# Optimization experiments

Measured on AMD Instinct MI355X. Metric: run time of the kernel, lower is better.

Reference implementation:

```python
import jax, jax.numpy as jnp
import numpy as np

EPS = 1e-5

def _ln(x, g, b):
    mu = jnp.mean(x, axis=-1, keepdims=True)
    var = jnp.var(x, axis=-1, keepdims=True)
    return (x - mu) * jax.lax.rsqrt(var + EPS) * g + b

def setup_inputs() -> dict:
    key = jax.random.key(0)
    ks = jax.random.split(key, 8)
    B, L, D, H = 2, 2048, 1024, 16
    F = 4096
    s = 0.02
    return {
        "x": jax.random.normal(ks[0], (B, L, D), dtype=jnp.float32),
        "attn_mask": jnp.tril(jnp.ones((L, L), dtype=jnp.float32)),
        # weights stored [in, out] (equivalent to torch Linear weight.T)
        "w_qkuv": jax.random.normal(ks[1], (D, 4 * D), dtype=jnp.float32) * s,
        "w_out": jax.random.normal(ks[2], (D, D), dtype=jnp.float32) * s,
        "w1": jax.random.normal(ks[3], (D, F), dtype=jnp.float32) * s,
        "w2": jax.random.normal(ks[4], (F, D), dtype=jnp.float32) * s,
        "w3": jax.random.normal(ks[5], (D, F), dtype=jnp.float32) * s,
        "ln1_g": jnp.ones((D,), jnp.float32), "ln1_b": jnp.zeros((D,), jnp.float32),
        "ln2_g": jnp.ones((D,), jnp.float32), "ln2_b": jnp.zeros((D,), jnp.float32),
        "na_g": jnp.ones((D // H,), jnp.float32), "na_b": jnp.zeros((D // H,), jnp.float32),
    }

def reference(x, attn_mask, w_qkuv, w_out, w1, w2, w3,
              ln1_g, ln1_b, ln2_g, ln2_b, na_g, na_b):
    B, L, D = x.shape
    H = 16
    d = D // H
    # --- SiLU attention sublayer ---
    xn = _ln(x, ln1_g, ln1_b)
    qkuv = jax.nn.silu(xn @ w_qkuv)                       # [B, L, 4D]
    q, k, v, u = jnp.split(qkuv, 4, axis=-1)
    def heads(t):
        return t.reshape(B, L, H, d).transpose(0, 2, 1, 3)  # [B, H, L, d]
    q, k, v, u = heads(q), heads(k), heads(v), heads(u)
    scores = jnp.einsum('bhqd,bhkd->bhqk', q, k) / jnp.sqrt(jnp.float32(d))
    scores = jax.nn.silu(scores) * attn_mask              # broadcast [L, L] over B, H
    a = jnp.einsum('bhqk,bhkd->bhqd', scores, v)          # [B, H, L, d]
    a = _ln(a, na_g, na_b) * u
    a = a.transpose(0, 2, 1, 3).reshape(B, L, D)
    x = x + a @ w_out
    # --- SwiGLU FFN sublayer ---
    xn2 = _ln(x, ln2_g, ln2_b)
    x = x + (jax.nn.silu(xn2 @ w1) * (xn2 @ w3)) @ w2
    return x
```

## Files before the change

kernel.cpp:

```cpp
#include <hip/hip_runtime.h>
#include <hip/hip_bf16.h>

typedef __hip_bfloat16 bf16;
typedef __attribute__((ext_vector_type(8))) short short8;
typedef __attribute__((ext_vector_type(4))) short bfv4;
typedef __attribute__((ext_vector_type(4))) float f32x4;
typedef __attribute__((ext_vector_type(4))) unsigned short us4;

#define LN_EPS 1e-5f

__device__ __forceinline__ float siluf(float x) { return x / (1.f + __expf(-x)); }
__device__ __forceinline__ unsigned short f2bf_bits(float f) {
    bf16 h = __float2bfloat16(f);
    return *reinterpret_cast<unsigned short*>(&h);
}
__device__ __forceinline__ bf16 f2bf(float f) { return __float2bfloat16(f); }
__device__ __forceinline__ float bf2f(bf16 h) { return __bfloat162float(h); }

__device__ __forceinline__ void load_lds16(const void* g, void* l) {
    __builtin_amdgcn_global_load_lds((const __attribute__((address_space(1))) void*)g,
                                     (__attribute__((address_space(3))) void*)l, 16, 0, 0);
}

__device__ __forceinline__ f32x4 mfma16(bfv4 a, bfv4 b, f32x4 c) {
    return __builtin_amdgcn_mfma_f32_16x16x16bf16_1k(a, b, c, 0, 0, 0);
}

__device__ __forceinline__ void drain_and_sync() {
    asm volatile("s_waitcnt vmcnt(0)" ::: "memory");
    __builtin_amdgcn_sched_barrier(0);
    __syncthreads();
}

template <int N>
__device__ __forceinline__ void wait_vmcnt() {
    asm volatile("s_waitcnt vmcnt(%0)" :: "n"(N) : "memory");
}
__device__ __forceinline__ void hard_barrier() {
    __builtin_amdgcn_sched_barrier(0);
    __builtin_amdgcn_s_barrier();
    __builtin_amdgcn_sched_barrier(0);
}
__device__ __forceinline__ void lgkm_barrier() {
    asm volatile("s_waitcnt lgkmcnt(0)" ::: "memory");
    __builtin_amdgcn_sched_barrier(0);
    __builtin_amdgcn_s_barrier();
    __builtin_amdgcn_sched_barrier(0);
}

__device__ __forceinline__ int xcd_swz(int bid, int nwg) {
    return (bid & 7) * (nwg >> 3) + (bid >> 3);
}

__global__ __launch_bounds__(256) void transpose_cast(
    const float* __restrict__ src, bf16* __restrict__ dst, int K, int N)
{
    __shared__ float t[32][33];
    const int nb = blockIdx.x << 5, kb = blockIdx.y << 5;
    const int tx = threadIdx.x, ty = threadIdx.y;
#pragma unroll
    for (int i = ty; i < 32; i += 8) t[i][tx] = src[(size_t)(kb + i) * N + nb + tx];
    __syncthreads();
#pragma unroll
    for (int i = ty; i < 32; i += 8) dst[(size_t)(nb + i) * K + kb + tx] = f2bf(t[tx][i]);
}

__global__ __launch_bounds__(256) void ln_cast(
    const float* __restrict__ x, const float* __restrict__ g, const float* __restrict__ be,
    bf16* __restrict__ out)
{
    const int row = blockIdx.x, tid = threadIdx.x;
    const float4 v = ((const float4*)(x + (size_t)row * 1024))[tid];
    float s = v.x + v.y + v.z + v.w;
    float ss = v.x * v.x + v.y * v.y + v.z * v.z + v.w * v.w;
#pragma unroll
    for (int o = 32; o; o >>= 1) { s += __shfl_down(s, o); ss += __shfl_down(ss, o); }
    __shared__ float red[10];
    const int wid = tid >> 6, lane = tid & 63;
    if (lane == 0) { red[wid] = s; red[4 + wid] = ss; }
    __syncthreads();
    if (tid == 0) {
        float S = red[0] + red[1] + red[2] + red[3];
        float SS = red[4] + red[5] + red[6] + red[7];
        float mu = S * (1.f / 1024.f);
        red[8] = mu;
        red[9] = rsqrtf(SS * (1.f / 1024.f) - mu * mu + LN_EPS);
    }
    __syncthreads();
    const float mu = red[8], rstd = red[9];
    const float4 gg = ((const float4*)g)[tid];
    const float4 bb = ((const float4*)be)[tid];
    us4 o;
    o[0] = f2bf_bits((v.x - mu) * rstd * gg.x + bb.x);
    o[1] = f2bf_bits((v.y - mu) * rstd * gg.y + bb.y);
    o[2] = f2bf_bits((v.z - mu) * rstd * gg.z + bb.z);
    o[3] = f2bf_bits((v.w - mu) * rstd * gg.w + bb.w);
    ((us4*)(out + (size_t)row * 1024))[tid] = o;
}

template <int EPI>
__global__ __launch_bounds__(512, 2) void gemm8(
    const bf16* __restrict__ A, const bf16* __restrict__ BT,
    bf16* __restrict__ outp, const bf16* __restrict__ mulsrc,
    int M, int N, int K)
{
    __shared__ __align__(16) bf16 lds[2][2][256 * 64];
    const int tid = threadIdx.x;
    const int wid = tid >> 6, lane = tid & 63;
    const int lhi = lane >> 4, llo = lane & 15;
    const int ntx = N >> 8;
    const int bid = xcd_swz((int)blockIdx.x, (int)gridDim.x);
    const int bx = bid % ntx, by = bid / ntx;
    const int row0 = by << 8, col0 = bx << 8;
    const int wr = wid >> 2, wc = wid & 3;
    const int wbase = wid << 6;

    auto stage_tile = [&](const bf16* src, int r0, int k0, char* ldsbase) {
#pragma unroll
        for (int it = 0; it < 4; ++it) {
            const int p = it * 512 + wbase + lane;
            const int r = p >> 3, pc = p & 7;
            const int lc = pc ^ (r & 7);
            load_lds16(src + (size_t)(r0 + r) * K + k0 + lc * 8,
                       ldsbase + (size_t)(it * 512 + wbase) * 16);
        }
    };
    auto stageA = [&](int t) { stage_tile(A, row0, t << 6, (char*)lds[t & 1][0]); };
    auto stageB = [&](int t) { stage_tile(BT, col0, t << 6, (char*)lds[t & 1][1]); };

    f32x4 acc[8][4] = {};

    stageA(0); stageB(0); stageA(1); stageB(1);
    wait_vmcnt<8>();
    hard_barrier();

    const int KT = K >> 6;
    for (int t = 0; t < KT; ++t) {
        const int buf = t & 1;
        const char* lAc = (const char*)lds[buf][0];
        const char* lBc = (const char*)lds[buf][1];

        short8 af[4], b0[2], b1[2];
        auto ldA = [&](int mh, int kk) {
#pragma unroll
            for (int m = 0; m < 4; ++m) {
                const int ra = wr * 128 + mh * 64 + m * 16 + llo;
                af[m] = *(const short8*)(lAc + ra * 128 + (((kk * 4 + lhi) ^ (ra & 7)) << 4));
            }
        };
        auto ldB = [&](short8* bf_, int nh, int kk) {
#pragma unroll
            for (int n = 0; n < 2; ++n) {
                const int rb = wc * 64 + nh * 32 + n * 16 + llo;
                bf_[n] = *(const short8*)(lBc + rb * 128 + (((kk * 4 + lhi) ^ (rb & 7)) << 4));
            }
        };
        auto mfma_q = [&](int mh, int nh, short8* bf_) {
            __builtin_amdgcn_s_setprio(1);
#pragma unroll
            for (int m = 0; m < 4; ++m)
#pragma unroll
                for (int n = 0; n < 2; ++n)
                    acc[mh * 4 + m][nh * 2 + n] =
                        __builtin_amdgcn_mfma_f32_16x16x32_bf16(af[m], bf_[n], acc[mh * 4 + m][nh * 2 + n], 0, 0, 0);
            __builtin_amdgcn_s_setprio(0);
        };

#pragma unroll
        for (int kk = 0; kk < 2; ++kk) {
            ldA(0, kk); ldB(b0, 0, kk);
            mfma_q(0, 0, b0);
            ldB(b1, 1, kk);
            mfma_q(0, 1, b1);
            ldA(1, kk);
            mfma_q(1, 0, b0);
            mfma_q(1, 1, b1);
        }

        lgkm_barrier();
        if (t + 2 < KT) {
            stageA(t + 2); stageB(t + 2);
            wait_vmcnt<8>();
            hard_barrier();
        } else if (t + 1 < KT) {
            wait_vmcnt<0>();
            hard_barrier();
        }
    }

#pragma unroll
    for (int m = 0; m < 8; ++m) {
        const int rbase = row0 + wr * 128 + m * 16 + lhi * 4;
#pragma unroll
        for (int n = 0; n < 4; ++n) {
            const int c = col0 + wc * 64 + n * 16 + llo;
#pragma unroll
            for (int r = 0; r < 4; ++r) {
                const size_t idx = (size_t)(rbase + r) * N + c;
                const float v = acc[m][n][r];
                if constexpr (EPI == 0) outp[idx] = f2bf(siluf(v));
                else                    outp[idx] = f2bf(v * bf2f(mulsrc[idx]));
            }
        }
    }
}

template <int EPI, int NF>
__global__ __launch_bounds__(256) void gemm_bt(
    const bf16* __restrict__ A, const bf16* __restrict__ BT,
    void* __restrict__ outp, const float* __restrict__ resid,
    int M, int N, int K)
{
    constexpr int BN = 32 * NF;
    __shared__ __align__(16) bf16 lA[2][128 * 32];
    __shared__ __align__(16) bf16 lB[2][BN * 32];
    const int tid = threadIdx.x;
    const int wid = tid >> 6, lane = tid & 63;
    const int lhi = lane >> 4, llo = lane & 15;
    const int ntx = N / BN;
    const int bid = xcd_swz((int)blockIdx.x, (int)gridDim.x);
    const int bx = bid % ntx, by = bid / ntx;
    const int row0 = by << 7, col0 = bx * BN;
    const int wr = wid >> 1, wc = wid & 1;
    const int wbase = wid << 6;
    f32x4 acc[4][NF] = {};

    auto stage = [&](int k0, int buf) {
        char* lAc = (char*)lA[buf];
        char* lBc = (char*)lB[buf];
#pragma unroll
        for (int i = 0; i < 2; ++i) {
            const int pe = i * 256 + wbase + lane;
            const int row = pe >> 2, pch = pe & 3;
            const int lch = pch ^ ((row >> 1) & 3);
            load_lds16(A + (size_t)(row0 + row) * K + k0 + lch * 8,
                       lAc + (size_t)(i * 256 + wbase) * 16);
        }
#pragma unroll
        for (int i = 0; i < NF / 2; ++i) {
            const int pe = i * 256 + wbase + lane;
            const int row = pe >> 2, pch = pe & 3;
            const int lch = pch ^ ((row >> 1) & 3);
            load_lds16(BT + (size_t)(col0 + row) * K + k0 + lch * 8,
                       lBc + (size_t)(i * 256 + wbase) * 16);
        }
    };

    stage(0, 0);
    const int KT = K >> 5;
    for (int kt = 0; kt < KT; ++kt) {
        const int cur = kt & 1;
        drain_and_sync();
        if (kt + 1 < KT) stage((kt + 1) << 5, cur ^ 1);
        const char* lAc = (const char*)lA[cur];
        const char* lBc = (const char*)lB[cur];
        short8 af[4], bfr[NF];
#pragma unroll
        for (int m = 0; m < 4; ++m) {
            const int ra = wr * 64 + m * 16 + llo;
            af[m] = *(const short8*)(lAc + ra * 64 + ((lhi ^ ((ra >> 1) & 3)) << 4));
        }
#pragma unroll
        for (int n = 0; n < NF; ++n) {
            const int rb = wc * (NF * 16) + n * 16 + llo;
            bfr[n] = *(const short8*)(lBc + rb * 64 + ((lhi ^ ((rb >> 1) & 3)) << 4));
        }
#pragma unroll
        for (int m = 0; m < 4; ++m)
#pragma unroll
            for (int n = 0; n < NF; ++n)
                acc[m][n] = __builtin_amdgcn_mfma_f32_16x16x32_bf16(af[m], bfr[n], acc[m][n], 0, 0, 0);
    }

#pragma unroll
    for (int m = 0; m < 4; ++m) {
        const int rbase = row0 + wr * 64 + m * 16 + lhi * 4;
#pragma unroll
        for (int n = 0; n < NF; ++n) {
            const int c = col0 + wc * (NF * 16) + n * 16 + llo;
#pragma unroll
            for (int r = 0; r < 4; ++r) {
                const size_t idx = (size_t)(rbase + r) * N + c;
                ((float*)outp)[idx] = resid[idx] + acc[m][n][r];
            }
        }
    }
}

__global__ __launch_bounds__(256) void v_trans(const bf16* __restrict__ qkuv, bf16* __restrict__ v_t)
{
    __shared__ bf16 t[64][65];
    const int bh = blockIdx.y;
    const int b = bh >> 4, h = bh & 15;
    const int l0 = blockIdx.x << 6;
    const int tx = threadIdx.x, ty = threadIdx.y;
#pragma unroll
    for (int i = ty; i < 64; i += 4)
        t[i][tx] = qkuv[(size_t)(b * 2048 + l0 + i) * 4096 + 2048 + h * 64 + tx];
    __syncthreads();
#pragma unroll
    for (int i = ty; i < 64; i += 4)
        v_t[(size_t)(bh * 64 + i) * 2048 + l0 + tx] = t[tx][i];
}

__global__ __launch_bounds__(512) void attn_kernel(
    const bf16* __restrict__ qkuv, const bf16* __restrict__ v_t,
    const float* __restrict__ nag, const float* __restrict__ nab,
    bf16* __restrict__ au)
{
    __shared__ __align__(16) bf16 lK[2][128 * 64];
    __shared__ __align__(16) bf16 lV[2][64 * 128];
    const int tid = threadIdx.x;
    const int wid = tid >> 6, lane = tid & 63;
    const int lhi = lane >> 4, llo = lane & 15;
    const int vb = xcd_swz((int)blockIdx.x, (int)gridDim.x);
    const int bh = vb >> 4;
    const int qt = 15 - (vb & 15);
    const int b = bh >> 4, h = bh & 15;
    const int q0 = qt << 7;
    const bf16* Qb = qkuv + (size_t)b * 2048 * 4096 + h * 64;
    const bf16* Kb = Qb + 1024;
    const bf16* Ub = Qb + 3072;
    const bf16* Vb = v_t + (size_t)bh * 64 * 2048;
    const int wbase = wid << 6;

    auto stage = [&](int kt_s, int buf) {
        const int koff = kt_s << 7;
        char* lKc = (char*)lK[buf];
        char* lVc = (char*)lV[buf];
#pragma unroll
        for (int it = 0; it < 2; ++it) {
            const int p = it * 512 + wbase + lane;
            const int r = p >> 3, pc = p & 7;
            const int lc = pc ^ (r & 7);
            load_lds16(Kb + (size_t)(koff + r) * 4096 + lc * 8, lKc + (it * 512 + wbase) * 16);
        }
#pragma unroll
        for (int it = 0; it < 2; ++it) {
            const int p = it * 512 + wbase + lane;
            const int d = p >> 4, pc = p & 15;
            const int lc = pc ^ (d & 15);
            load_lds16(Vb + (size_t)d * 2048 + koff + lc * 8, lVc + (it * 512 + wbase) * 16);
        }
    };

    short8 qb[2];
#pragma unroll
    for (int kk = 0; kk < 2; ++kk)
        qb[kk] = *(const short8*)(Qb + (size_t)(q0 + wid * 16 + llo) * 4096 + kk * 32 + lhi * 8);

    f32x4 acc2[4] = {};

    stage(0, 0);

    for (int kt = 0; kt <= qt; ++kt) {
        const int cur = kt & 1;
        drain_and_sync();
        if (kt < qt) stage(kt + 1, cur ^ 1);
        const char* lKc = (const char*)lK[cur];
        const char* lVc = (const char*)lV[cur];

        const bool diag = (kt == qt);
#pragma unroll
        for (int m = 0; m < 8; ++m) {
            if (diag && m > wid) break;
            const int rK = m * 16 + llo;
            const int sw = rK & 7;
            short8 ak0 = *(const short8*)(lKc + rK * 128 + ((lhi ^ sw) << 4));
            short8 ak1 = *(const short8*)(lKc + rK * 128 + (((4 + lhi) ^ sw) << 4));
            f32x4 s = {};
            s = __builtin_amdgcn_mfma_f32_16x16x32_bf16(ak0, qb[0], s, 0, 0, 0);
            s = __builtin_amdgcn_mfma_f32_16x16x32_bf16(ak1, qb[1], s, 0, 0, 0);
            const bool mask = diag && (m == wid);
            bfv4 a16;
#pragma unroll
            for (int r = 0; r < 4; ++r) {
                float xx = s[r] * 0.125f;
                xx = xx * __builtin_amdgcn_rcpf(1.f + __expf(-xx));
                if (mask && (lhi * 4 + r > llo)) xx = 0.f;
                a16[r] = (short)f2bf_bits(xx);
            }
#pragma unroll
            for (int dcol = 0; dcol < 4; ++dcol) {
                const int d = dcol * 16 + llo;
                const int lcV = m * 2 + (lhi >> 1);
                bfv4 bv = *(const bfv4*)(lVc + d * 256 + ((lcV ^ llo) << 4) + (lhi & 1) * 8);
                acc2[dcol] = mfma16(a16, bv, acc2[dcol]);
            }
        }
    }

#pragma unroll
    for (int r = 0; r < 4; ++r) {
        float vv[4];
        float s = 0.f, ss = 0.f;
#pragma unroll
        for (int dc = 0; dc < 4; ++dc) { vv[dc] = acc2[dc][r]; s += vv[dc]; ss += vv[dc] * vv[dc]; }
#pragma unroll
        for (int o = 1; o < 16; o <<= 1) { s += __shfl_xor(s, o); ss += __shfl_xor(ss, o); }
        const float mu = s * (1.f / 64.f);
        const float rstd = rsqrtf(ss * (1.f / 64.f) - mu * mu + LN_EPS);
        const int q = wid * 16 + lhi * 4 + r;
        const size_t grow = q0 + q;
#pragma unroll
        for (int dc = 0; dc < 4; ++dc) {
            const int c = dc * 16 + llo;
            const float nv = (vv[dc] - mu) * rstd * nag[c] + nab[c];
            const float uu = bf2f(Ub[grow * 4096 + c]);
            au[(size_t)(b * 2048 + grow) * 1024 + h * 64 + c] = f2bf(nv * uu);
        }
    }
}

extern "C" void kernel_launch(void* const* d_in, const int* in_sizes, int n_in,
                              void* d_out, int out_size, void* d_ws, size_t ws_size,
                              hipStream_t stream)
{
    const float* x      = (const float*)d_in[0];
    const float* w_qkuv = (const float*)d_in[2];
    const float* w_out  = (const float*)d_in[3];
    const float* w1     = (const float*)d_in[4];
    const float* w2     = (const float*)d_in[5];
    const float* w3     = (const float*)d_in[6];
    const float* ln1g   = (const float*)d_in[7];
    const float* ln1b   = (const float*)d_in[8];
    const float* ln2g   = (const float*)d_in[9];
    const float* ln2b   = (const float*)d_in[10];
    const float* nag    = (const float*)d_in[11];
    const float* nab    = (const float*)d_in[12];
    float* out = (float*)d_out;

    char* ws = (char*)d_ws;
    size_t off = 0;
    auto alloc = [&](size_t bytes) { void* p = ws + off; off += (bytes + 255) & ~(size_t)255; return p; };
    const size_t M = 4096;
    bf16* wqkuvT = (bf16*)alloc(4096ull * 1024 * 2);
    bf16* woutT  = (bf16*)alloc(1024ull * 1024 * 2);
    bf16* w1T    = (bf16*)alloc(4096ull * 1024 * 2);
    bf16* w3T    = (bf16*)alloc(4096ull * 1024 * 2);
    bf16* w2T    = (bf16*)alloc(1024ull * 4096 * 2);
    bf16* xn     = (bf16*)alloc(M * 1024 * 2);
    bf16* qkuv   = (bf16*)alloc(M * 4096 * 2);
    bf16* vt     = (bf16*)alloc(32ull * 64 * 2048 * 2);
    bf16* aub    = (bf16*)alloc(M * 1024 * 2);
    float* x2    = (float*)alloc(M * 1024 * 4);
    bf16* xn2    = (bf16*)alloc(M * 1024 * 2);
    bf16* g1     = (bf16*)alloc(M * 4096 * 2);
    bf16* h1     = (bf16*)alloc(M * 4096 * 2);
    (void)ws_size; (void)in_sizes; (void)n_in; (void)out_size;

    dim3 tb(32, 8);
    transpose_cast<<<dim3(4096 / 32, 1024 / 32), tb, 0, stream>>>(w_qkuv, wqkuvT, 1024, 4096);
    transpose_cast<<<dim3(1024 / 32, 1024 / 32), tb, 0, stream>>>(w_out, woutT, 1024, 1024);
    transpose_cast<<<dim3(4096 / 32, 1024 / 32), tb, 0, stream>>>(w1, w1T, 1024, 4096);
    transpose_cast<<<dim3(4096 / 32, 1024 / 32), tb, 0, stream>>>(w3, w3T, 1024, 4096);
    transpose_cast<<<dim3(1024 / 32, 4096 / 32), tb, 0, stream>>>(w2, w2T, 4096, 1024);

    ln_cast<<<M, 256, 0, stream>>>(x, ln1g, ln1b, xn);

    gemm8<0><<<dim3((M / 256) * (4096 / 256)), 512, 0, stream>>>(xn, wqkuvT, qkuv, nullptr, M, 4096, 1024);

    v_trans<<<dim3(2048 / 64, 32), dim3(64, 4), 0, stream>>>(qkuv, vt);

    attn_kernel<<<dim3(512), 512, 0, stream>>>(qkuv, vt, nag, nab, aub);

    gemm_bt<1, 2><<<dim3((M / 128) * (1024 / 64)), 256, 0, stream>>>(aub, woutT, x2, x, M, 1024, 1024);

    ln_cast<<<M, 256, 0, stream>>>(x2, ln2g, ln2b, xn2);

    gemm8<0><<<dim3((M / 256) * (4096 / 256)), 512, 0, stream>>>(xn2, w1T, g1, nullptr, M, 4096, 1024);
    gemm8<2><<<dim3((M / 256) * (4096 / 256)), 512, 0, stream>>>(xn2, w3T, h1, g1, M, 4096, 1024);

    gemm_bt<1, 2><<<dim3((M / 128) * (1024 / 64)), 256, 0, stream>>>(h1, w2T, out, x2, M, 1024, 4096);
}
```

Baseline: 331.5 us.

## Deepen residual GEMM pipeline with BK=64 tiles and prefetch-two-ahead staging

Replaces the residual-add GEMM used for the out-projection and w2 down-projection with a version that uses 64-wide K tiles, an 8-chunk XOR swizzle, and stages tiles two iterations ahead using explicit vmcnt waits instead of a full drain each step. It also raises wave priority around the MFMA block. The aim is to cut per-iteration barrier and load-latency stalls and to halve the number of K iterations. The cost is twice the LDS per block, which may lower occupancy. Prefetching two tiles ahead into a two-slot buffer also relies on careful barrier ordering to avoid overwriting a buffer that is still being read.

New measurement: 322.3 us. -2.8%, faster.

```diff
diff --git a/kernel.cpp b/kernel.cpp
--- a/kernel.cpp
+++ b/kernel.cpp
@@ -205,83 +205,98 @@
     }
 }
 
-template <int EPI, int NF>
-__global__ __launch_bounds__(256) void gemm_bt(
+__global__ __launch_bounds__(256) void gemm_btc(
     const bf16* __restrict__ A, const bf16* __restrict__ BT,
-    void* __restrict__ outp, const float* __restrict__ resid,
+    float* __restrict__ outp, const float* __restrict__ resid,
     int M, int N, int K)
 {
-    constexpr int BN = 32 * NF;
-    __shared__ __align__(16) bf16 lA[2][128 * 32];
-    __shared__ __align__(16) bf16 lB[2][BN * 32];
+    __shared__ __align__(16) bf16 lA[2][128 * 64];
+    __shared__ __align__(16) bf16 lB[2][64 * 64];
     const int tid = threadIdx.x;
     const int wid = tid >> 6, lane = tid & 63;
     const int lhi = lane >> 4, llo = lane & 15;
-    const int ntx = N / BN;
+    const int ntx = N >> 6;
     const int bid = xcd_swz((int)blockIdx.x, (int)gridDim.x);
     const int bx = bid % ntx, by = bid / ntx;
-    const int row0 = by << 7, col0 = bx * BN;
+    const int row0 = by << 7, col0 = bx << 6;
     const int wr = wid >> 1, wc = wid & 1;
     const int wbase = wid << 6;
-    f32x4 acc[4][NF] = {};
-
-    auto stage = [&](int k0, int buf) {
-        char* lAc = (char*)lA[buf];
-        char* lBc = (char*)lB[buf];
-#pragma unroll
-        for (int i = 0; i < 2; ++i) {
-            const int pe = i * 256 + wbase + lane;
-            const int row = pe >> 2, pch = pe & 3;
-            const int lch = pch ^ ((row >> 1) & 3);
-            load_lds16(A + (size_t)(row0 + row) * K + k0 + lch * 8,
-                       lAc + (size_t)(i * 256 + wbase) * 16);
-        }
-#pragma unroll
-        for (int i = 0; i < NF / 2; ++i) {
-            const int pe = i * 256 + wbase + lane;
-            const int row = pe >> 2, pch = pe & 3;
-            const int lch = pch ^ ((row >> 1) & 3);
-            load_lds16(BT + (size_t)(col0 + row) * K + k0 + lch * 8,
-                       lBc + (size_t)(i * 256 + wbase) * 16);
+
+    auto stage_tile = [&](const bf16* src, int r0, int k0, char* ldsbase, int nit) {
+        for (int it = 0; it < nit; ++it) {
+            const int p = it * 256 + wbase + lane;
+            const int r = p >> 3, pc = p & 7;
+            const int lc = pc ^ (r & 7);
+            load_lds16(src + (size_t)(r0 + r) * K + k0 + lc * 8,
+                       ldsbase + (size_t)(it * 256 + wbase) * 16);
         }
     };
-
-    stage(0, 0);
-    const int KT = K >> 5;
-    for (int kt = 0; kt < KT; ++kt) {
-        const int cur = kt & 1;
-        drain_and_sync();
-        if (kt + 1 < KT) stage((kt + 1) << 5, cur ^ 1);
-        const char* lAc = (const char*)lA[cur];
-        const char* lBc = (const char*)lB[cur];
-        short8 af[4], bfr[NF];
-#pragma unroll
-        for (int m = 0; m < 4; ++m) {
-            const int ra = wr * 64 + m * 16 + llo;
-            af[m] = *(const short8*)(lAc + ra * 64 + ((lhi ^ ((ra >> 1) & 3)) << 4));
-        }
-#pragma unroll
-        for (int n = 0; n < NF; ++n) {
-            const int rb = wc * (NF * 16) + n * 16 + llo;
-            bfr[n] = *(const short8*)(lBc + rb * 64 + ((lhi ^ ((rb >> 1) & 3)) << 4));
-        }
-#pragma unroll
-        for (int m = 0; m < 4; ++m)
-#pragma unroll
-            for (int n = 0; n < NF; ++n)
-                acc[m][n] = __builtin_amdgcn_mfma_f32_16x16x32_bf16(af[m], bfr[n], acc[m][n], 0, 0, 0);
+    auto stageT = [&](int t) {
+        stage_tile(A, row0, t << 6, (char*)lA[t & 1], 4);
+        stage_tile(BT, col0, t << 6, (char*)lB[t & 1], 2);
+    };
+
+    f32x4 acc[4][2] = {};
+
+    stageT(0); stageT(1);
+    wait_vmcnt<6>();
+    hard_barrier();
+
+    const int KT = K >> 6;
+    for (int t = 0; t < KT; ++t) {
+        const int buf = t & 1;
+        const char* lAc = (const char*)lA[buf];
+        const char* lBc = (const char*)lB[buf];
+
+        short8 af[4], bfr[2];
+        auto ldA = [&](int kk) {
+#pragma unroll
+            for (int m = 0; m < 4; ++m) {
+                const int ra = wr * 64 + m * 16 + llo;
+                af[m] = *(const short8*)(lAc + ra * 128 + (((kk * 4 + lhi) ^ (ra & 7)) << 4));
+            }
+        };
+        auto ldB = [&](int kk) {
+#pragma unroll
+            for (int n = 0; n < 2; ++n) {
+                const int rb = wc * 32 + n * 16 + llo;
+                bfr[n] = *(const short8*)(lBc + rb * 128 + (((kk * 4 + lhi) ^ (rb & 7)) << 4));
+            }
+        };
+
+#pragma unroll
+        for (int kk = 0; kk < 2; ++kk) {
+            ldA(kk); ldB(kk);
+            __builtin_amdgcn_s_setprio(1);
+#pragma unroll
+            for (int m = 0; m < 4; ++m)
+#pragma unroll
+                for (int n = 0; n < 2; ++n)
+                    acc[m][n] = __builtin_amdgcn_mfma_f32_16x16x32_bf16(af[m], bfr[n], acc[m][n], 0, 0, 0);
+            __builtin_amdgcn_s_setprio(0);
+        }
+
+        lgkm_barrier();
+        if (t + 2 < KT) {
+            stageT(t + 2);
+            wait_vmcnt<6>();
+            hard_barrier();
+        } else if (t + 1 < KT) {
+            wait_vmcnt<0>();
+            hard_barrier();
+        }
     }
 
 #pragma unroll
     for (int m = 0; m < 4; ++m) {
         const int rbase = row0 + wr * 64 + m * 16 + lhi * 4;
 #pragma unroll
-        for (int n = 0; n < NF; ++n) {
-            const int c = col0 + wc * (NF * 16) + n * 16 + llo;
+        for (int n = 0; n < 2; ++n) {
+            const int c = col0 + wc * 32 + n * 16 + llo;
 #pragma unroll
             for (int r = 0; r < 4; ++r) {
                 const size_t idx = (size_t)(rbase + r) * N + c;
-                ((float*)outp)[idx] = resid[idx] + acc[m][n][r];
+                outp[idx] = resid[idx] + acc[m][n][r];
             }
         }
     }
@@ -464,12 +479,12 @@
 
     attn_kernel<<<dim3(512), 512, 0, stream>>>(qkuv, vt, nag, nab, aub);
 
-    gemm_bt<1, 2><<<dim3((M / 128) * (1024 / 64)), 256, 0, stream>>>(aub, woutT, x2, x, M, 1024, 1024);
+    gemm_btc<<<dim3((M / 128) * (1024 / 64)), 256, 0, stream>>>(aub, woutT, x2, x, M, 1024, 1024);
 
     ln_cast<<<M, 256, 0, stream>>>(x2, ln2g, ln2b, xn2);
 
     gemm8<0><<<dim3((M / 256) * (4096 / 256)), 512, 0, stream>>>(xn2, w1T, g1, nullptr, M, 4096, 1024);
     gemm8<2><<<dim3((M / 256) * (4096 / 256)), 512, 0, stream>>>(xn2, w3T, h1, g1, M, 4096, 1024);
 
-    gemm_bt<1, 2><<<dim3((M / 128) * (1024 / 64)), 256, 0, stream>>>(h1, w2T, out, x2, M, 1024, 4096);
-}
+    gemm_btc<<<dim3((M / 128) * (1024 / 64)), 256, 0, stream>>>(h1, w2T, out, x2, M, 1024, 4096);
+}
```
